# Kernel tuning notes

Measured on AMD Instinct MI355X. Metric: run time of the kernel, lower is better.

The kernel has to match this reference:

```python
import jax, jax.numpy as jnp
import numpy as np

B, S, D, H = 8, 2048, 1024, 16
HD = D // H  # head_dim = 64


def setup_inputs() -> dict:
    key = jax.random.key(0)
    ks = jax.random.split(key, 10)
    s = 0.02
    return {
        "x": jax.random.normal(ks[0], (B, S, D), jnp.float32),
        "mask": jnp.zeros((B, 1, S), jnp.float32),
        "Wq": jax.random.normal(ks[1], (D, D), jnp.float32) * s,
        "bq": jnp.zeros((D,), jnp.float32),
        "Wk": jax.random.normal(ks[2], (D, D), jnp.float32) * s,
        "bk": jnp.zeros((D,), jnp.float32),
        "Wv": jax.random.normal(ks[3], (D, D), jnp.float32) * s,
        "bv": jnp.zeros((D,), jnp.float32),
        "wa": jax.random.normal(ks[4], (HD, 1), jnp.float32) * s,
        "ba": jnp.zeros((1,), jnp.float32),
        "wb": jax.random.normal(ks[5], (HD, 1), jnp.float32) * s,
        "bb": jnp.zeros((1,), jnp.float32),
        "Wu": jax.random.normal(ks[6], (HD, HD), jnp.float32) * s,
        "bu": jnp.zeros((HD,), jnp.float32),
        "Wo": jax.random.normal(ks[7], (D, D), jnp.float32) * s,
        "bo": jnp.zeros((D,), jnp.float32),
        "gamma": jnp.ones((D,), jnp.float32),
        "beta_ln": jnp.zeros((D,), jnp.float32),
    }


def _split_heads(t):
    # [B,S,D] -> [B,H,S,HD]
    return t.reshape(B, S, H, HD).transpose(0, 2, 1, 3)


def reference(x, mask, Wq, bq, Wk, bk, Wv, bv, wa, ba, wb, bb, Wu, bu, Wo, bo, gamma, beta_ln):
    scale = 1.0 / jnp.sqrt(jnp.float32(HD))
    q = _split_heads(x @ Wq + bq)  # [B,H,S,HD]
    k = _split_heads(x @ Wk + bk)
    v = _split_heads(x @ Wv + bv)

    # additive attention over queries -> global query vector per head
    alphascore = (jnp.squeeze(q @ wa, -1) + ba[0]) * scale + mask  # [B,H,S]
    alphaw = jax.nn.softmax(alphascore, axis=-1)
    q_av = jnp.einsum('bhs,bhsd->bhd', alphaw, q)

    p = k * q_av[:, :, None, :]  # gated keys [B,H,S,HD]
    betascore = (jnp.squeeze(p @ wb, -1) + bb[0]) * scale + mask
    betaw = jax.nn.softmax(betascore, axis=-1)
    p_av = jnp.einsum('bhs,bhsd->bhd', betaw, p)

    u = v * p_av[:, :, None, :]  # gated values
    r = u @ Wu + bu  # [B,H,S,HD]
    newr = (r + q).transpose(0, 2, 1, 3).reshape(B, S, D)
    attn_out = newr @ Wo + bo

    h = x + attn_out
    mu = jnp.mean(h, axis=-1, keepdims=True)
    var = jnp.mean(jnp.square(h - mu), axis=-1, keepdims=True)
    return (h - mu) * jax.lax.rsqrt(var + 1e-6) * gamma + beta_ln
```

## Files before the change

kernel.cpp:

```cpp
#include <hip/hip_runtime.h>
#include <cstdint>

#define BB 8
#define SS 2048
#define DD 1024
#define HH 16
#define HDIM 64
#define MTOT (BB*SS)
#define NQKV 3072

typedef __attribute__((ext_vector_type(8))) __bf16 bf16x8;
typedef __attribute__((ext_vector_type(4))) float f32x4;

#define AS1(p) ((const __attribute__((address_space(1))) void*)(p))
#define AS3(p) ((__attribute__((address_space(3))) void*)(p))

__device__ __forceinline__ float bf2f(uint16_t u){
  return __uint_as_float(((uint32_t)u) << 16);
}
__device__ __forceinline__ uint16_t f2bf(float f){
  uint32_t u = __float_as_uint(f);
  return (uint16_t)((u + 0x7fffu + ((u >> 16) & 1u)) >> 16);
}

__global__ __launch_bounds__(256)
void k_prep(const float* __restrict__ x,
            const float* __restrict__ Wq, const float* __restrict__ Wk,
            const float* __restrict__ Wv, const float* __restrict__ Wo,
            const float* __restrict__ bq, const float* __restrict__ bk,
            const float* __restrict__ bv,
            uint16_t* __restrict__ xb, uint16_t* __restrict__ Wt,
            uint16_t* __restrict__ WoT, float* __restrict__ bqkv)
{
  __shared__ float t[32][33];
  const int blk = blockIdx.x, tid = threadIdx.x;
  if (blk < 2048){
    const int n4 = MTOT*DD/4;
    for (int i = blk*256 + tid; i < n4; i += 2048*256){
      float4 v = reinterpret_cast<const float4*>(x)[i];
      ushort4 o;
      o.x = f2bf(v.x); o.y = f2bf(v.y); o.z = f2bf(v.z); o.w = f2bf(v.w);
      reinterpret_cast<ushort4*>(xb)[i] = o;
    }
  } else if (blk < 6144){
    const int zb = blk - 2048;
    const int z = zb >> 10, rem = zb & 1023;
    const int by = rem >> 5, bx = rem & 31;
    const float* src = (z==0)?Wq:(z==1)?Wk:(z==2)?Wv:Wo;
    uint16_t* dst = (z<3) ? (Wt + (size_t)z*1024*1024) : WoT;
    const int k0 = by*32, n0 = bx*32;
    const int tx = tid & 31, ty = tid >> 5;
    #pragma unroll
    for (int r = 0; r < 4; ++r)
      t[ty + r*8][tx] = src[(size_t)(k0 + ty + r*8)*1024 + n0 + tx];
    __syncthreads();
    #pragma unroll
    for (int r = 0; r < 4; ++r)
      dst[(size_t)(n0 + ty + r*8)*1024 + k0 + tx] = f2bf(t[tx][ty + r*8]);
  } else {
    const int i = (blk - 6144)*256 + tid;
    if (i < NQKV)
      bqkv[i] = (i < 1024) ? bq[i] : (i < 2048) ? bk[i-1024] : bv[i-2048];
  }
}


#define BARRIER __builtin_amdgcn_s_barrier()
#define LGKM0 { asm volatile("s_waitcnt lgkmcnt(0)" ::: "memory"); __builtin_amdgcn_sched_barrier(0); }

#define READA(BUF, MH) { \
  const uint16_t* _sl = lds + ((BUF)*4 + (MH))*8192; \
  _Pragma("unroll") \
  for (int f = 0; f < 4; ++f){ \
    const int lr = wm*64 + f*16 + l15; \
    _Pragma("unroll") \
    for (int ks = 0; ks < 2; ++ks){ \
      const int pu = (ks*4 + l4) ^ l7; \
      a[f][ks] = *(const bf16x8*)(_sl + lr*64 + pu*8); \
    } \
  } }

#define READB(BUF, NH) { \
  const uint16_t* _sl = lds + ((BUF)*4 + 2 + (NH))*8192; \
  _Pragma("unroll") \
  for (int j = 0; j < 2; ++j){ \
    const int lr = wn*32 + j*16 + l15; \
    _Pragma("unroll") \
    for (int ks = 0; ks < 2; ++ks){ \
      const int pu = (ks*4 + l4) ^ l7; \
      b[j][ks] = *(const bf16x8*)(_sl + lr*64 + pu*8); \
    } \
  } }

#define MMA(MH, NH) { \
  __builtin_amdgcn_s_setprio(1); \
  _Pragma("unroll") \
  for (int ks = 0; ks < 2; ++ks) \
    _Pragma("unroll") \
    for (int f = 0; f < 4; ++f) \
      _Pragma("unroll") \
      for (int j = 0; j < 2; ++j) \
        acc[(MH)*4+f][(NH)*2+j] = __builtin_amdgcn_mfma_f32_16x16x32_bf16(a[f][ks], b[j][ks], acc[(MH)*4+f][(NH)*2+j], 0, 0, 0); \
  __builtin_amdgcn_s_setprio(0); }

#define STAGEA(T, H) { \
  const int _kt = (T); \
  const int _gid = swz + ((_kt>>4)<<8); \
  const int _m0s = (_gid/NB_T)<<8; \
  const int _c0s = (_kt&15)<<6; \
  char* _d = (char*)lds + (((_kt)&1)*4 + (H))*16384 + wave*1024; \
  _Pragma("unroll") \
  for (int l = 0; l < 2; ++l){ \
    const int lr = l*64 + (tid>>3); \
    const int r = _m0s + ((lr>>6)<<7) + ((H)<<6) + (lr&63); \
    const int c = _c0s + (((tid&7) ^ (lr&7)) << 3); \
    __builtin_amdgcn_global_load_lds(AS1(A + (size_t)r*K + c), AS3(_d + l*8192), 16, 0, 0); \
  } }

#define STAGEB(T, H) { \
  const int _kt = (T); \
  const int _gid = swz + ((_kt>>4)<<8); \
  const int _n0s = (_gid%NB_T)<<8; \
  const int _c0s = (_kt&15)<<6; \
  char* _d = (char*)lds + (((_kt)&1)*4 + 2 + (H))*16384 + wave*1024; \
  _Pragma("unroll") \
  for (int l = 0; l < 2; ++l){ \
    const int lr = l*64 + (tid>>3); \
    const int r = _n0s + ((lr>>5)<<6) + ((H)<<5) + (lr&31); \
    const int c = _c0s + (((tid&7) ^ (lr&7)) << 3); \
    __builtin_amdgcn_global_load_lds(AS1(Bt + (size_t)r*K + c), AS3(_d + l*8192), 16, 0, 0); \
  } }

#define CWRITE(TAU) { \
  const int _gid = swz + ((TAU)<<8); \
  const int _m0c = (_gid/NB_T)<<8, _n0c = (_gid%NB_T)<<8; \
  _Pragma("unroll") \
  for (int mh = 0; mh < 2; ++mh) \
  _Pragma("unroll") \
  for (int f = 0; f < 4; ++f) \
  _Pragma("unroll") \
  for (int nh = 0; nh < 2; ++nh) \
  _Pragma("unroll") \
  for (int j = 0; j < 2; ++j){ \
    const int gcol = _n0c + wn*64 + nh*32 + j*16 + l15; \
    const float bi = bias[gcol]; \
    const int rbase = _m0c + wm*128 + mh*64 + f*16 + l4*4; \
    _Pragma("unroll") \
    for (int rr = 0; rr < 4; ++rr){ \
      const size_t idx = (size_t)(rbase + rr)*N + gcol; \
      float v = acc[mh*4+f][nh*2+j][rr] + bi; \
      if (EPI == 1) v += bf2f(resid16[idx]); \
      Cout[idx] = f2bf(v); \
    } \
  } }

template<int EPI, int NB_T>
__global__ __launch_bounds__(512, 2)
void k_gemm256(const uint16_t* __restrict__ A, const uint16_t* __restrict__ Bt,
               const float* __restrict__ bias, const uint16_t* __restrict__ resid16,
               uint16_t* __restrict__ Cout, int M, int N, int K, int TPB)
{
  __shared__ uint16_t lds[8 * 8192];
  const int tid = threadIdx.x;
  const int lane = tid & 63, wave = tid >> 6;
  const int wm = wave >> 2, wn = wave & 3;
  const int l15 = lane & 15, l4 = lane >> 4, l7 = lane & 7;

  const int bid = blockIdx.x;
  const int swz = (bid & 7) * 32 + (bid >> 3);

  f32x4 acc[8][4] = {};
  bf16x8 a[4][2], b[2][2];

  const int nTot = TPB * 8;

  STAGEA(0,0); STAGEB(0,1); STAGEA(0,1); STAGEB(0,0);
  STAGEA(1,0); STAGEB(1,1); STAGEA(1,1);
  asm volatile("s_waitcnt vmcnt(6)" ::: "memory");
  BARRIER;

  #pragma unroll 1
  for (int I = 0; I < nTot - 1; ++I){
    const int e = 2*I;
    READA(0,0); READB(0,0); STAGEB(e+1, 0);
    BARRIER; LGKM0; MMA(0,0); BARRIER;
    READB(0,1); STAGEA(e+2, 0);
    BARRIER; LGKM0; MMA(0,1); BARRIER;
    READA(0,1); STAGEB(e+2, 1);
    BARRIER; LGKM0; MMA(1,1); BARRIER;
    READB(0,0); STAGEA(e+2, 1);
    asm volatile("s_waitcnt vmcnt(6)" ::: "memory");
    BARRIER; LGKM0; MMA(1,0); BARRIER;
    READA(1,0); READB(1,0); STAGEB(e+2, 0);
    BARRIER; LGKM0; MMA(0,0); BARRIER;
    READB(1,1); STAGEA(e+3, 0);
    BARRIER; LGKM0; MMA(0,1); BARRIER;
    READA(1,1); STAGEB(e+3, 1);
    BARRIER; LGKM0; MMA(1,1); BARRIER;
    READB(1,0); STAGEA(e+3, 1);
    asm volatile("s_waitcnt vmcnt(6)" ::: "memory");
    BARRIER; LGKM0; MMA(1,0); BARRIER;
    if ((I & 7) == 7){
      CWRITE(I >> 3);
      #pragma unroll
      for (int p = 0; p < 8; ++p)
        #pragma unroll
        for (int q = 0; q < 4; ++q)
          acc[p][q] = (f32x4){0.f,0.f,0.f,0.f};
    }
  }

  {
    const int e = 2*nTot - 2;
    READA(0,0); READB(0,0); STAGEB(e+1, 0);
    BARRIER; LGKM0; MMA(0,0); BARRIER;
    READB(0,1);
    BARRIER; LGKM0; MMA(0,1); BARRIER;
    READA(0,1);
    BARRIER; LGKM0; MMA(1,1); BARRIER;
    READB(0,0);
    asm volatile("s_waitcnt vmcnt(0)" ::: "memory");
    BARRIER; LGKM0; MMA(1,0); BARRIER;
    READA(1,0); READB(1,0);
    BARRIER; LGKM0; MMA(0,0); BARRIER;
    READB(1,1);
    BARRIER; LGKM0; MMA(0,1); BARRIER;
    READA(1,1);
    BARRIER; LGKM0; MMA(1,1); BARRIER;
    READB(1,0);
    BARRIER; LGKM0; MMA(1,0); BARRIER;
  }
  CWRITE(TPB - 1);
}

__device__ __forceinline__ float block_red_max512(float v, float* red, int tid){
  red[tid] = v; __syncthreads();
  for (int off = 256; off > 0; off >>= 1){
    if (tid < off) red[tid] = fmaxf(red[tid], red[tid+off]);
    __syncthreads();
  }
  float r = red[0]; __syncthreads();
  return r;
}
__device__ __forceinline__ float block_red_sum512(float v, float* red, int tid){
  red[tid] = v; __syncthreads();
  for (int off = 256; off > 0; off >>= 1){
    if (tid < off) red[tid] += red[tid+off];
    __syncthreads();
  }
  float r = red[0]; __syncthreads();
  return r;
}

__device__ __forceinline__ void score_pass(const uint16_t* __restrict__ base,
    float biasv, const float* wv, float* sc, const float* __restrict__ mrow, int tid){
  for (int s = tid; s < SS; s += 512){
    const uint16_t* row = base + (size_t)s*NQKV;
    float acc = 0.f;
    #pragma unroll
    for (int jj = 0; jj < 8; ++jj){
      int4 raw = *(const int4*)(row + jj*8);
      unsigned uu[4] = {(unsigned)raw.x,(unsigned)raw.y,(unsigned)raw.z,(unsigned)raw.w};
      #pragma unroll
      for (int e = 0; e < 4; ++e){
        acc += __uint_as_float(uu[e] << 16)        * wv[jj*8 + 2*e]
             + __uint_as_float(uu[e] & 0xffff0000u) * wv[jj*8 + 2*e + 1];
      }
    }
    sc[s] = (acc + biasv)*0.125f + mrow[s];
  }
}

__device__ __forceinline__ void col_accum(const uint16_t* __restrict__ base,
    const float* sc, float part[8][64], int tid){
  const int j = tid & 63, g = tid >> 6;
  const uint16_t* p = base + (size_t)(g*256)*NQKV + j;
  float a = 0.f;
  for (int s = 0; s < 256; ++s)
    a += sc[g*256 + s] * bf2f(p[(size_t)s*NQKV]);
  part[g][j] = a;
}

__global__ __launch_bounds__(512)
void k_head(const uint16_t* __restrict__ qkv, const float* __restrict__ mask,
            const float* __restrict__ wa, const float* __restrict__ ba,
            const float* __restrict__ wb, const float* __restrict__ bbp,
            const float* __restrict__ Wu, uint16_t* __restrict__ WuPT)
{
  __shared__ float sc[SS];
  __shared__ float red[512];
  __shared__ float part[8][64];
  __shared__ float qav[64];
  __shared__ float wvec[64];
  __shared__ float pav[64];

  const int bh = blockIdx.x, b = bh >> 4, h = bh & 15;
  const int tid = threadIdx.x;
  const uint16_t* qb  = qkv + (size_t)b*SS*NQKV + h*64;
  const uint16_t* kb2 = qb + 1024;
  const float* mrow = mask + b*SS;

  if (tid < 64) wvec[tid] = wa[tid];
  __syncthreads();

  score_pass(qb, ba[0], wvec, sc, mrow, tid);
  __syncthreads();
  float lm = -3.4e38f;
  for (int s = tid; s < SS; s += 512) lm = fmaxf(lm, sc[s]);
  float mx = block_red_max512(lm, red, tid);
  float ls = 0.f;
  for (int s = tid; s < SS; s += 512){ float e = __expf(sc[s]-mx); sc[s] = e; ls += e; }
  __syncthreads();
  float inv = 1.f / block_red_sum512(ls, red, tid);

  col_accum(qb, sc, part, tid);
  __syncthreads();
  if (tid < 64){
    float q = 0.f;
    #pragma unroll
    for (int g = 0; g < 8; ++g) q += part[g][tid];
    qav[tid] = q*inv;
    wvec[tid] = q*inv*wb[tid];
  }
  __syncthreads();

  score_pass(kb2, bbp[0], wvec, sc, mrow, tid);
  __syncthreads();
  lm = -3.4e38f;
  for (int s = tid; s < SS; s += 512) lm = fmaxf(lm, sc[s]);
  mx = block_red_max512(lm, red, tid);
  ls = 0.f;
  for (int s = tid; s < SS; s += 512){ float e = __expf(sc[s]-mx); sc[s] = e; ls += e; }
  __syncthreads();
  float inv2 = 1.f / block_red_sum512(ls, red, tid);

  col_accum(kb2, sc, part, tid);
  __syncthreads();
  if (tid < 64){
    float p = 0.f;
    #pragma unroll
    for (int g = 0; g < 8; ++g) p += part[g][tid];
    pav[tid] = qav[tid]*p*inv2;
  }
  __syncthreads();

  uint16_t* dst = WuPT + (size_t)bh*4096;
  for (int idx = tid; idx < 4096; idx += 512){
    const int i = idx & 63, jcol = idx >> 6;
    dst[idx] = f2bf(pav[i]*Wu[i*64 + jcol]);
  }
}

__global__ __launch_bounds__(256)
void k_newr(const uint16_t* __restrict__ qkv, const uint16_t* __restrict__ WuPT,
            const float* __restrict__ bu, uint16_t* __restrict__ newr)
{
  const int bh = blockIdx.x >> 3, st = blockIdx.x & 7;
  const int b = bh >> 4, h = bh & 15;
  const int tid = threadIdx.x, wave = tid >> 6, lane = tid & 63;
  const int l15 = lane & 15, l4 = lane >> 4;
  const int s0 = st*256 + wave*64;
  const uint16_t* vb = qkv + 2048 + h*64;
  const uint16_t* wt = WuPT + (size_t)bh*4096;

  f32x4 acc[4][4] = {};
  #pragma unroll
  for (int ks = 0; ks < 2; ++ks){
    bf16x8 bfr[4];
    #pragma unroll
    for (int n = 0; n < 4; ++n)
      bfr[n] = *(const bf16x8*)(wt + (n*16 + l15)*64 + ks*32 + l4*8);
    #pragma unroll
    for (int m = 0; m < 4; ++m){
      const int s = s0 + m*16 + l15;
      bf16x8 af = *(const bf16x8*)(vb + (size_t)(b*SS + s)*NQKV + ks*32 + l4*8);
      #pragma unroll
      for (int n = 0; n < 4; ++n)
        acc[m][n] = __builtin_amdgcn_mfma_f32_16x16x32_bf16(af, bfr[n], acc[m][n], 0, 0, 0);
    }
  }
  #pragma unroll
  for (int n = 0; n < 4; ++n){
    const int j = n*16 + l15;
    const float bj = bu[j];
    #pragma unroll
    for (int m = 0; m < 4; ++m){
      #pragma unroll
      for (int r = 0; r < 4; ++r){
        const int s = s0 + m*16 + l4*4 + r;
        const size_t qidx = (size_t)(b*SS + s)*NQKV + h*64 + j;
        const float q = bf2f(qkv[qidx]);
        newr[(size_t)(b*SS + s)*DD + h*64 + j] = f2bf(acc[m][n][r] + bj + q);
      }
    }
  }
}

__global__ __launch_bounds__(256)
void k_ln(const uint16_t* __restrict__ h16, const float* __restrict__ gamma,
          const float* __restrict__ beta, float* __restrict__ out)
{
  __shared__ float r1[256], r2[256];
  const int row = blockIdx.x, tid = threadIdx.x;
  const ushort4 hv = ((const ushort4*)(h16 + (size_t)row*DD))[tid];
  float v0 = bf2f(hv.x), v1 = bf2f(hv.y), v2 = bf2f(hv.z), v3 = bf2f(hv.w);
  float s  = v0 + v1 + v2 + v3;
  float ss = v0*v0 + v1*v1 + v2*v2 + v3*v3;
  r1[tid] = s; r2[tid] = ss; __syncthreads();
  for (int off = 128; off > 0; off >>= 1){
    if (tid < off){ r1[tid] += r1[tid+off]; r2[tid] += r2[tid+off]; }
    __syncthreads();
  }
  const float mu  = r1[0]*(1.f/1024.f);
  const float var = r2[0]*(1.f/1024.f) - mu*mu;
  const float inv = rsqrtf(var + 1e-6f);
  const float4 g  = ((const float4*)gamma)[tid];
  const float4 be = ((const float4*)beta)[tid];
  float4 o;
  o.x = (v0-mu)*inv*g.x + be.x;
  o.y = (v1-mu)*inv*g.y + be.y;
  o.z = (v2-mu)*inv*g.z + be.z;
  o.w = (v3-mu)*inv*g.w + be.w;
  ((float4*)(out + (size_t)row*DD))[tid] = o;
}

extern "C" void kernel_launch(void* const* d_in, const int* in_sizes, int n_in,
                              void* d_out, int out_size, void* d_ws, size_t ws_size,
                              hipStream_t stream) {
  const float* x    = (const float*)d_in[0];
  const float* mask = (const float*)d_in[1];
  const float* Wq   = (const float*)d_in[2];
  const float* bq   = (const float*)d_in[3];
  const float* Wk   = (const float*)d_in[4];
  const float* bk   = (const float*)d_in[5];
  const float* Wv   = (const float*)d_in[6];
  const float* bv   = (const float*)d_in[7];
  const float* wa   = (const float*)d_in[8];
  const float* ba   = (const float*)d_in[9];
  const float* wb   = (const float*)d_in[10];
  const float* bb   = (const float*)d_in[11];
  const float* Wu   = (const float*)d_in[12];
  const float* bu   = (const float*)d_in[13];
  const float* Wo   = (const float*)d_in[14];
  const float* bo   = (const float*)d_in[15];
  const float* gamma= (const float*)d_in[16];
  const float* beta = (const float*)d_in[17];
  float* out = (float*)d_out;

  char* ws = (char*)d_ws;
  const size_t MB = 1ull << 20;
  uint16_t* xb    = (uint16_t*)(ws);
  uint16_t* Wt    = (uint16_t*)(ws + 32*MB);
  uint16_t* WoT   = (uint16_t*)(ws + 38*MB);
  float*    bqkv  = (float*)   (ws + 40*MB);
  uint16_t* WuPT  = (uint16_t*)(ws + 41*MB);
  uint16_t* qkv   = (uint16_t*)(ws + 42*MB);
  uint16_t* newr  = (uint16_t*)(ws + 138*MB);
  uint16_t* hbuf16= (uint16_t*)(ws + 42*MB);

  k_prep<<<6156, 256, 0, stream>>>(x, Wq, Wk, Wv, Wo, bq, bk, bv, xb, Wt, WoT, bqkv);

  k_gemm256<0,12><<<256, 512, 0, stream>>>(xb, Wt, bqkv, nullptr, qkv,
                                           MTOT, NQKV, DD, 3);
  k_head<<<BB*HH, 512, 0, stream>>>(qkv, mask, wa, ba, wb, bb, Wu, WuPT);
  k_newr<<<BB*HH*8, 256, 0, stream>>>(qkv, WuPT, bu, newr);
  k_gemm256<1,4><<<256, 512, 0, stream>>>(newr, WoT, bo, xb, hbuf16,
                                          MTOT, DD, DD, 1);
  k_ln<<<MTOT, 256, 0, stream>>>(hbuf16, gamma, beta, out);
}
```

Baseline: 262.9 us.

## Switch GEMM from persistent multi-tile blocks to one tile per workgroup

The GEMM kernel previously ran 256 persistent workgroups, each looping over several output tiles. It now launches one workgroup per 256x256 tile and fully unrolls a fixed K loop of 1024. Global addresses are precomputed once as base pointers plus constant offsets, and two B register sets let the last MMA reuse b0 instead of reloading it from LDS. This cuts per-stage address arithmetic and LDS reads, at the cost of more launched workgroups and the loss of persistent-tile reuse and of the occupancy hint.

```diff
diff --git a/kernel.cpp b/kernel.cpp
--- a/kernel.cpp
+++ b/kernel.cpp
@@ -71,28 +71,22 @@
 #define READA(BUF, MH) { \
   const uint16_t* _sl = lds + ((BUF)*4 + (MH))*8192; \
   _Pragma("unroll") \
-  for (int f = 0; f < 4; ++f){ \
-    const int lr = wm*64 + f*16 + l15; \
+  for (int f = 0; f < 4; ++f) \
     _Pragma("unroll") \
-    for (int ks = 0; ks < 2; ++ks){ \
-      const int pu = (ks*4 + l4) ^ l7; \
-      a[f][ks] = *(const bf16x8*)(_sl + lr*64 + pu*8); \
-    } \
-  } }
-
-#define READB(BUF, NH) { \
+    for (int ks = 0; ks < 2; ++ks) \
+      a[f][ks] = *(const bf16x8*)(_sl + (wm*64 + f*16 + l15)*64 + (((ks*4 + l4) ^ l7)<<3)); \
+}
+
+#define READB(BUF, NH, BV) { \
   const uint16_t* _sl = lds + ((BUF)*4 + 2 + (NH))*8192; \
   _Pragma("unroll") \
-  for (int j = 0; j < 2; ++j){ \
-    const int lr = wn*32 + j*16 + l15; \
+  for (int j = 0; j < 2; ++j) \
     _Pragma("unroll") \
-    for (int ks = 0; ks < 2; ++ks){ \
-      const int pu = (ks*4 + l4) ^ l7; \
-      b[j][ks] = *(const bf16x8*)(_sl + lr*64 + pu*8); \
-    } \
-  } }
-
-#define MMA(MH, NH) { \
+    for (int ks = 0; ks < 2; ++ks) \
+      BV[j][ks] = *(const bf16x8*)(_sl + (wn*32 + j*16 + l15)*64 + (((ks*4 + l4) ^ l7)<<3)); \
+}
+
+#define MMA(MH, NH, BV) { \
   __builtin_amdgcn_s_setprio(1); \
   _Pragma("unroll") \
   for (int ks = 0; ks < 2; ++ks) \
@@ -100,137 +94,112 @@
     for (int f = 0; f < 4; ++f) \
       _Pragma("unroll") \
       for (int j = 0; j < 2; ++j) \
-        acc[(MH)*4+f][(NH)*2+j] = __builtin_amdgcn_mfma_f32_16x16x32_bf16(a[f][ks], b[j][ks], acc[(MH)*4+f][(NH)*2+j], 0, 0, 0); \
+        acc[(MH)*4+f][(NH)*2+j] = __builtin_amdgcn_mfma_f32_16x16x32_bf16(a[f][ks], BV[j][ks], acc[(MH)*4+f][(NH)*2+j], 0, 0, 0); \
   __builtin_amdgcn_s_setprio(0); }
 
 #define STAGEA(T, H) { \
-  const int _kt = (T); \
-  const int _gid = swz + ((_kt>>4)<<8); \
-  const int _m0s = (_gid/NB_T)<<8; \
-  const int _c0s = (_kt&15)<<6; \
-  char* _d = (char*)lds + (((_kt)&1)*4 + (H))*16384 + wave*1024; \
+  char* _d = (char*)lds + ((((T)&1)*4 + (H))*16384) + wave*1024; \
   _Pragma("unroll") \
-  for (int l = 0; l < 2; ++l){ \
-    const int lr = l*64 + (tid>>3); \
-    const int r = _m0s + ((lr>>6)<<7) + ((H)<<6) + (lr&63); \
-    const int c = _c0s + (((tid&7) ^ (lr&7)) << 3); \
-    __builtin_amdgcn_global_load_lds(AS1(A + (size_t)r*K + c), AS3(_d + l*8192), 16, 0, 0); \
-  } }
+  for (int l = 0; l < 2; ++l) \
+    __builtin_amdgcn_global_load_lds(AS1(pA + (l*131072 + (H)*65536 + (T)*64)), AS3(_d + l*8192), 16, 0, 0); \
+}
 
 #define STAGEB(T, H) { \
-  const int _kt = (T); \
-  const int _gid = swz + ((_kt>>4)<<8); \
-  const int _n0s = (_gid%NB_T)<<8; \
-  const int _c0s = (_kt&15)<<6; \
-  char* _d = (char*)lds + (((_kt)&1)*4 + 2 + (H))*16384 + wave*1024; \
+  char* _d = (char*)lds + ((((T)&1)*4 + 2 + (H))*16384) + wave*1024; \
   _Pragma("unroll") \
-  for (int l = 0; l < 2; ++l){ \
-    const int lr = l*64 + (tid>>3); \
-    const int r = _n0s + ((lr>>5)<<6) + ((H)<<5) + (lr&31); \
-    const int c = _c0s + (((tid&7) ^ (lr&7)) << 3); \
-    __builtin_amdgcn_global_load_lds(AS1(Bt + (size_t)r*K + c), AS3(_d + l*8192), 16, 0, 0); \
-  } }
-
-#define CWRITE(TAU) { \
-  const int _gid = swz + ((TAU)<<8); \
-  const int _m0c = (_gid/NB_T)<<8, _n0c = (_gid%NB_T)<<8; \
-  _Pragma("unroll") \
-  for (int mh = 0; mh < 2; ++mh) \
-  _Pragma("unroll") \
-  for (int f = 0; f < 4; ++f) \
-  _Pragma("unroll") \
-  for (int nh = 0; nh < 2; ++nh) \
-  _Pragma("unroll") \
-  for (int j = 0; j < 2; ++j){ \
-    const int gcol = _n0c + wn*64 + nh*32 + j*16 + l15; \
-    const float bi = bias[gcol]; \
-    const int rbase = _m0c + wm*128 + mh*64 + f*16 + l4*4; \
-    _Pragma("unroll") \
-    for (int rr = 0; rr < 4; ++rr){ \
-      const size_t idx = (size_t)(rbase + rr)*N + gcol; \
-      float v = acc[mh*4+f][nh*2+j][rr] + bi; \
-      if (EPI == 1) v += bf2f(resid16[idx]); \
-      Cout[idx] = f2bf(v); \
-    } \
-  } }
+  for (int l = 0; l < 2; ++l) \
+    __builtin_amdgcn_global_load_lds(AS1(pB + (l*131072 + (H)*32768 + (T)*64)), AS3(_d + l*8192), 16, 0, 0); \
+}
 
 template<int EPI, int NB_T>
-__global__ __launch_bounds__(512, 2)
+__global__ __launch_bounds__(512)
 void k_gemm256(const uint16_t* __restrict__ A, const uint16_t* __restrict__ Bt,
                const float* __restrict__ bias, const uint16_t* __restrict__ resid16,
-               uint16_t* __restrict__ Cout, int M, int N, int K, int TPB)
+               uint16_t* __restrict__ Cout)
 {
+  constexpr int N = NB_T * 256;
   __shared__ uint16_t lds[8 * 8192];
   const int tid = threadIdx.x;
   const int lane = tid & 63, wave = tid >> 6;
   const int wm = wave >> 2, wn = wave & 3;
   const int l15 = lane & 15, l4 = lane >> 4, l7 = lane & 7;
 
-  const int bid = blockIdx.x;
-  const int swz = (bid & 7) * 32 + (bid >> 3);
+  const int nwg = gridDim.x, cpx = nwg >> 3, bid = blockIdx.x;
+  const int wg = (bid & 7) * cpx + (bid >> 3);
+  const int m0 = (wg / NB_T) << 8, n0 = (wg % NB_T) << 8;
+
+  const int colbase = (((tid & 7) ^ ((tid >> 3) & 7)) << 3);
+  const uint16_t* pA = A  + (size_t)(m0 + (tid >> 3)) * 1024 + colbase;
+  const uint16_t* pB = Bt + (size_t)(n0 + ((tid >> 8) << 6) + ((tid >> 3) & 31)) * 1024 + colbase;
 
   f32x4 acc[8][4] = {};
-  bf16x8 a[4][2], b[2][2];
-
-  const int nTot = TPB * 8;
+  bf16x8 a[4][2], b0[2][2], b1[2][2];
 
   STAGEA(0,0); STAGEB(0,1); STAGEA(0,1); STAGEB(0,0);
   STAGEA(1,0); STAGEB(1,1); STAGEA(1,1);
   asm volatile("s_waitcnt vmcnt(6)" ::: "memory");
   BARRIER;
 
-  #pragma unroll 1
-  for (int I = 0; I < nTot - 1; ++I){
+  #pragma unroll
+  for (int I = 0; I < 7; ++I){
     const int e = 2*I;
-    READA(0,0); READB(0,0); STAGEB(e+1, 0);
-    BARRIER; LGKM0; MMA(0,0); BARRIER;
-    READB(0,1); STAGEA(e+2, 0);
-    BARRIER; LGKM0; MMA(0,1); BARRIER;
+    READA(0,0); READB(0,0,b0); STAGEB(e+1, 0);
+    BARRIER; LGKM0; MMA(0,0,b0); BARRIER;
+    READB(0,1,b1); STAGEA(e+2, 0);
+    BARRIER; LGKM0; MMA(0,1,b1); BARRIER;
     READA(0,1); STAGEB(e+2, 1);
-    BARRIER; LGKM0; MMA(1,1); BARRIER;
-    READB(0,0); STAGEA(e+2, 1);
+    BARRIER; LGKM0; MMA(1,1,b1); BARRIER;
+    STAGEA(e+2, 1);
     asm volatile("s_waitcnt vmcnt(6)" ::: "memory");
-    BARRIER; LGKM0; MMA(1,0); BARRIER;
-    READA(1,0); READB(1,0); STAGEB(e+2, 0);
-    BARRIER; LGKM0; MMA(0,0); BARRIER;
-    READB(1,1); STAGEA(e+3, 0);
-    BARRIER; LGKM0; MMA(0,1); BARRIER;
+    BARRIER; LGKM0; MMA(1,0,b0); BARRIER;
+    READA(1,0); READB(1,0,b0); STAGEB(e+2, 0);
+    BARRIER; LGKM0; MMA(0,0,b0); BARRIER;
+    READB(1,1,b1); STAGEA(e+3, 0);
+    BARRIER; LGKM0; MMA(0,1,b1); BARRIER;
     READA(1,1); STAGEB(e+3, 1);
-    BARRIER; LGKM0; MMA(1,1); BARRIER;
-    READB(1,0); STAGEA(e+3, 1);
+    BARRIER; LGKM0; MMA(1,1,b1); BARRIER;
+    STAGEA(e+3, 1);
     asm volatile("s_waitcnt vmcnt(6)" ::: "memory");
-    BARRIER; LGKM0; MMA(1,0); BARRIER;
-    if ((I & 7) == 7){
-      CWRITE(I >> 3);
-      #pragma unroll
-      for (int p = 0; p < 8; ++p)
-        #pragma unroll
-        for (int q = 0; q < 4; ++q)
-          acc[p][q] = (f32x4){0.f,0.f,0.f,0.f};
+    BARRIER; LGKM0; MMA(1,0,b0); BARRIER;
+  }
+
+  {
+    READA(0,0); READB(0,0,b0); STAGEB(15, 0);
+    BARRIER; LGKM0; MMA(0,0,b0); BARRIER;
+    READB(0,1,b1);
+    BARRIER; LGKM0; MMA(0,1,b1); BARRIER;
+    READA(0,1);
+    BARRIER; LGKM0; MMA(1,1,b1); BARRIER;
+    asm volatile("s_waitcnt vmcnt(0)" ::: "memory");
+    BARRIER; LGKM0; MMA(1,0,b0); BARRIER;
+    READA(1,0); READB(1,0,b0);
+    BARRIER; LGKM0; MMA(0,0,b0); BARRIER;
+    READB(1,1,b1);
+    BARRIER; LGKM0; MMA(0,1,b1); BARRIER;
+    READA(1,1);
+    BARRIER; LGKM0; MMA(1,1,b1); BARRIER;
+    LGKM0; MMA(1,0,b0);
+  }
+
+  #pragma unroll
+  for (int mh = 0; mh < 2; ++mh)
+  #pragma unroll
+  for (int f = 0; f < 4; ++f)
+  #pragma unroll
+  for (int nh = 0; nh < 2; ++nh)
+  #pragma unroll
+  for (int j = 0; j < 2; ++j){
+    const int gcol = n0 + wn*64 + nh*32 + j*16 + l15;
+    const float bi = bias[gcol];
+    const int rbase = m0 + wm*128 + mh*64 + f*16 + l4*4;
+    #pragma unroll
+    for (int rr = 0; rr < 4; ++rr){
+      const size_t idx = (size_t)(rbase + rr)*N + gcol;
+      float v = acc[mh*4+f][nh*2+j][rr] + bi;
+      if (EPI == 1) v += bf2f(resid16[idx]);
+      Cout[idx] = f2bf(v);
     }
   }
-
-  {
-    const int e = 2*nTot - 2;
-    READA(0,0); READB(0,0); STAGEB(e+1, 0);
-    BARRIER; LGKM0; MMA(0,0); BARRIER;
-    READB(0,1);
-    BARRIER; LGKM0; MMA(0,1); BARRIER;
-    READA(0,1);
-    BARRIER; LGKM0; MMA(1,1); BARRIER;
-    READB(0,0);
-    asm volatile("s_waitcnt vmcnt(0)" ::: "memory");
-    BARRIER; LGKM0; MMA(1,0); BARRIER;
-    READA(1,0); READB(1,0);
-    BARRIER; LGKM0; MMA(0,0); BARRIER;
-    READB(1,1);
-    BARRIER; LGKM0; MMA(0,1); BARRIER;
-    READA(1,1);
-    BARRIER; LGKM0; MMA(1,1); BARRIER;
-    READB(1,0);
-    BARRIER; LGKM0; MMA(1,0); BARRIER;
-  }
-  CWRITE(TPB - 1);
 }
 
 __device__ __forceinline__ float block_red_max512(float v, float* red, int tid){
@@ -460,11 +429,9 @@
 
   k_prep<<<6156, 256, 0, stream>>>(x, Wq, Wk, Wv, Wo, bq, bk, bv, xb, Wt, WoT, bqkv);
 
-  k_gemm256<0,12><<<256, 512, 0, stream>>>(xb, Wt, bqkv, nullptr, qkv,
-                                           MTOT, NQKV, DD, 3);
+  k_gemm256<0,12><<<(MTOT/256)*(NQKV/256), 512, 0, stream>>>(xb, Wt, bqkv, nullptr, qkv);
   k_head<<<BB*HH, 512, 0, stream>>>(qkv, mask, wa, ba, wb, bb, Wu, WuPT);
   k_newr<<<BB*HH*8, 256, 0, stream>>>(qkv, WuPT, bu, newr);
-  k_gemm256<1,4><<<256, 512, 0, stream>>>(newr, WoT, bo, xb, hbuf16,
-                                          MTOT, DD, DD, 1);
+  k_gemm256<1,4><<<(MTOT/256)*(DD/256), 512, 0, stream>>>(newr, WoT, bo, xb, hbuf16);
   k_ln<<<MTOT, 256, 0, stream>>>(hbuf16, gamma, beta, out);
 }
```

Result: faster. 254.9 us (-3.0%).
